# Kernel tuning notes

Hardware: AMD Instinct MI355X
Metric: run time of the kernel (lower is better)

## Reference

```python
import jax, jax.numpy as jnp
import numpy as np

DIM = 512
HEADS = 8
HEAD_DIM = DIM // HEADS
SCALE = HEAD_DIM ** -0.5
GROUP1 = np.array([2, 3, 5, 6, 1, 4, 0, 7, 8, 9, 14, 15, 11, 12, 10, 13])
GROUP2 = np.array([0, 1, 2, 3, 5, 6, 4, 7])
EPS = 1e-5


def setup_inputs() -> dict:
    key = jax.random.key(0)
    ks = jax.random.split(key, 6)
    B, N, C = 4096, 16, DIM
    x = jax.random.normal(ks[0], (B, N, C), dtype=jnp.float32)
    w_q = jax.random.normal(ks[1], (C, C), dtype=jnp.float32) * 0.02
    w_kv = jax.random.normal(ks[2], (2 * C, C), dtype=jnp.float32) * 0.02
    w_proj = jax.random.normal(ks[3], (C, C), dtype=jnp.float32) * 0.02
    b_proj = jax.random.normal(ks[4], (C,), dtype=jnp.float32) * 0.02
    gamma = jnp.ones((C,), dtype=jnp.float32)
    beta = jnp.zeros((C,), dtype=jnp.float32)
    return {"x": x, "w_q": w_q, "w_kv": w_kv, "w_proj": w_proj,
            "b_proj": b_proj, "gamma": gamma, "beta": beta}


def _layernorm(x, gamma, beta):
    mu = jnp.mean(x, axis=-1, keepdims=True)
    var = jnp.mean(jnp.square(x - mu), axis=-1, keepdims=True)
    return (x - mu) * jax.lax.rsqrt(var + EPS) * gamma + beta


def _avg_pool_pairs(x):
    # x: (B, L, C) -> (B, L//2, C), AvgPool1d(kernel=2, stride=2) over L
    return 0.5 * (x[:, 0::2] + x[:, 1::2])


def reference(x, w_q, w_kv, w_proj, b_proj, gamma, beta):
    B, N, C = x.shape
    q = (x @ w_q.T).reshape(B, N, HEADS, HEAD_DIM).transpose(0, 2, 1, 3)  # (B,H,N,d)
    # gather + avgpool preprocessing
    p1 = _avg_pool_pairs(x[:, GROUP1])  # (B, 8, C)
    p2 = _avg_pool_pairs(x[:, GROUP2])  # (B, 4, C)
    pools = jnp.concatenate([x, p1, p2], axis=1)  # (B, N+12, C)
    pools = _layernorm(pools, gamma, beta)
    M = pools.shape[1]
    kv = (pools @ w_kv.T).reshape(B, M, 2, HEADS, HEAD_DIM).transpose(2, 0, 3, 1, 4)
    k, v = kv[0], kv[1]  # (B,H,M,d)
    attn = jax.nn.softmax(jnp.einsum('bhnd,bhmd->bhnm', q, k) * SCALE, axis=-1)
    out = jnp.einsum('bhnm,bhmd->bhnd', attn, v)  # (B,H,N,d)
    out = out.transpose(0, 2, 1, 3).reshape(B, N, C)
    return out @ w_proj.T + b_proj
```

## Files before the change

kernel.cpp:

```cpp
#include <hip/hip_runtime.h>
#include <hip/hip_bf16.h>
#include <cstdint>
#include <cstddef>


using bf16 = __hip_bfloat16;

#define B_SZ   4096
#define NTOK   16
#define CDIM   512
#define MPOOL  28
#define NHEAD  8
#define HDIM   64
#define LN_EPS 1e-5f
#define ATT_SCALE 0.125f

typedef short bf16x8 __attribute__((ext_vector_type(8)));
typedef float f32x4  __attribute__((ext_vector_type(4)));

__constant__ int c_g1[16] = {2,3,5,6,1,4,0,7,8,9,14,15,11,12,10,13};
__constant__ int c_g2[8]  = {0,1,2,3,5,6,4,7};

__device__ __forceinline__ float us2f(unsigned short u) {
    return __uint_as_float(((unsigned)u) << 16);
}
__device__ __forceinline__ unsigned short f2b(float f) {
    unsigned u = __float_as_uint(f);
    return (unsigned short)((u + 0x7FFFu + ((u >> 16) & 1u)) >> 16);
}

__device__ __forceinline__ void lds_cp16(const void* g, void* l) {
    __builtin_amdgcn_global_load_lds(
        (const __attribute__((address_space(1))) void*)g,
        (__attribute__((address_space(3))) void*)l, 16, 0, 0);
}

__global__ __launch_bounds__(256) void f32_to_bf16_kernel(
    const float* __restrict__ src, bf16* __restrict__ dst, int n8)
{
    const int i = blockIdx.x * 256 + threadIdx.x;
    if (i >= n8) return;
    const float4* p = (const float4*)(src + (size_t)i * 8);
    float4 a = p[0], b = p[1];
    uint4 pk;
    pk.x = (unsigned)f2b(a.x) | ((unsigned)f2b(a.y) << 16);
    pk.y = (unsigned)f2b(a.z) | ((unsigned)f2b(a.w) << 16);
    pk.z = (unsigned)f2b(b.x) | ((unsigned)f2b(b.y) << 16);
    pk.w = (unsigned)f2b(b.z) | ((unsigned)f2b(b.w) << 16);
    *(uint4*)(dst + (size_t)i * 8) = pk;
}

__global__ __launch_bounds__(256) void pools_ln_kernel(
    const float* __restrict__ x, const float* __restrict__ gamma,
    const float* __restrict__ beta, bf16* __restrict__ pools,
    bf16* __restrict__ xb)
{
    const int wave = threadIdx.x >> 6;
    const int lane = threadIdx.x & 63;
    const int row  = blockIdx.x * 4 + wave;
    const int b = row / MPOOL;
    const int m = row % MPOOL;
    const float* xb_src = x + (size_t)b * NTOK * CDIM;
    const int c0 = lane * 8;

    float v[8];
    if (m < 16) {
        const float4* p = (const float4*)(xb_src + m * CDIM + c0);
        float4 a = p[0], c = p[1];
        v[0]=a.x; v[1]=a.y; v[2]=a.z; v[3]=a.w;
        v[4]=c.x; v[5]=c.y; v[6]=c.z; v[7]=c.w;
        uint4 pk;
        pk.x = (unsigned)f2b(v[0]) | ((unsigned)f2b(v[1]) << 16);
        pk.y = (unsigned)f2b(v[2]) | ((unsigned)f2b(v[3]) << 16);
        pk.z = (unsigned)f2b(v[4]) | ((unsigned)f2b(v[5]) << 16);
        pk.w = (unsigned)f2b(v[6]) | ((unsigned)f2b(v[7]) << 16);
        *(uint4*)(xb + (size_t)b * NTOK * CDIM + (size_t)m * CDIM + c0) = pk;
    } else {
        int r0, r1;
        if (m < 24) { int j = m - 16; r0 = c_g1[2*j]; r1 = c_g1[2*j+1]; }
        else        { int j = m - 24; r0 = c_g2[2*j]; r1 = c_g2[2*j+1]; }
        const float4* p0 = (const float4*)(xb_src + r0 * CDIM + c0);
        const float4* p1 = (const float4*)(xb_src + r1 * CDIM + c0);
        float4 a0 = p0[0], a1 = p0[1];
        float4 b0 = p1[0], b1 = p1[1];
        v[0]=0.5f*(a0.x+b0.x); v[1]=0.5f*(a0.y+b0.y);
        v[2]=0.5f*(a0.z+b0.z); v[3]=0.5f*(a0.w+b0.w);
        v[4]=0.5f*(a1.x+b1.x); v[5]=0.5f*(a1.y+b1.y);
        v[6]=0.5f*(a1.z+b1.z); v[7]=0.5f*(a1.w+b1.w);
    }

    float s = 0.f, sq = 0.f;
#pragma unroll
    for (int j = 0; j < 8; ++j) { s += v[j]; sq += v[j]*v[j]; }
#pragma unroll
    for (int off = 1; off < 64; off <<= 1) {
        s  += __shfl_xor(s,  off, 64);
        sq += __shfl_xor(sq, off, 64);
    }
    const float mu   = s * (1.f / CDIM);
    const float var  = sq * (1.f / CDIM) - mu * mu;
    const float rstd = rsqrtf(var + LN_EPS);

    unsigned short o[8];
#pragma unroll
    for (int j = 0; j < 8; ++j) {
        float g  = gamma[c0 + j];
        float bb = beta[c0 + j];
        o[j] = f2b((v[j] - mu) * rstd * g + bb);
    }
    uint4 pk;
    pk.x = (unsigned)o[0] | ((unsigned)o[1] << 16);
    pk.y = (unsigned)o[2] | ((unsigned)o[3] << 16);
    pk.z = (unsigned)o[4] | ((unsigned)o[5] << 16);
    pk.w = (unsigned)o[6] | ((unsigned)o[7] << 16);
    *(uint4*)(pools + (size_t)row * CDIM + c0) = pk;
}

template<bool OUT_BF16, bool BIAS, int NBLK>
__global__ __launch_bounds__(512, 2) void gemm256_kernel(
    const bf16* __restrict__ A, const bf16* __restrict__ W,
    const float* __restrict__ bias, void* __restrict__ Cptr, int Ncols)
{
    constexpr int K  = 512;
    constexpr int NT = K / 32;
    extern __shared__ __align__(16) char ring[];

    const int tid = threadIdx.x;
    const int wv = tid >> 6, ln = tid & 63;
    const int wr = wv >> 2, wc = wv & 3;
    const int fr = ln & 15, kb = ln >> 4;

    const int p  = blockIdx.x;
    const int o  = p >> 3;
    const int mb = (o / NBLK) * 8 + (p & 7);
    const int nb = o % NBLK;
    const size_t m0 = (size_t)mb * 256;
    const size_t n0 = (size_t)nb * 256;

    const int srow = wv * 16 + (ln >> 2);
    const int scol = (((ln & 3) * 16) ^ (((ln >> 3) & 3) << 4)) >> 1;
    const bf16* Asrc0 = A + (m0 + srow) * K + scol;
    const bf16* Asrc1 = A + (m0 + 128 + srow) * K + scol;
    const bf16* Wsrc0 = W + (n0 + srow) * K + scol;
    const bf16* Wsrc1 = W + (n0 + 128 + srow) * K + scol;
    char* const ringc = ring;

    const int aswz  = ((fr >> 1) & 3) << 4;
    const int a_off = (wr * 128 + fr) * 64 + ((kb * 16) ^ aswz);
    const int b_off = 16384 + (wc * 64 + fr) * 64 + ((kb * 16) ^ aswz);

    f32x4 acc[8][4];
#pragma unroll
    for (int i = 0; i < 8; ++i)
#pragma unroll
    for (int j = 0; j < 4; ++j)
        acc[i][j] = f32x4{0.f, 0.f, 0.f, 0.f};

    auto STAGE = [&](int t) {
        char* base = ringc + (t & 3) * 32768 + wv * 1024;
        const int ko = t * 32;
        lds_cp16(Asrc0 + ko, base);
        lds_cp16(Asrc1 + ko, base + 8192);
        lds_cp16(Wsrc0 + ko, base + 16384);
        lds_cp16(Wsrc1 + ko, base + 16384 + 8192);
    };

    STAGE(0);
    STAGE(1);
    asm volatile("s_waitcnt vmcnt(4)" ::: "memory");
    __builtin_amdgcn_s_barrier();

#pragma unroll 1
    for (int t = 0; t < NT; ++t) {
        if (t + 2 < NT) STAGE(t + 2);
        const char* sa = ringc + (t & 3) * 32768;

        bf16x8 af[8], bfr[4];
#pragma unroll
        for (int mi = 0; mi < 8; ++mi)
            af[mi] = *(const bf16x8*)(sa + a_off + mi * 1024);
#pragma unroll
        for (int nj = 0; nj < 4; ++nj)
            bfr[nj] = *(const bf16x8*)(sa + b_off + nj * 1024);

#pragma unroll
        for (int mi = 0; mi < 8; ++mi)
#pragma unroll
        for (int nj = 0; nj < 4; ++nj)
            acc[mi][nj] = __builtin_amdgcn_mfma_f32_16x16x32_bf16(
                af[mi], bfr[nj], acc[mi][nj], 0, 0, 0);

        if (t + 2 < NT) { asm volatile("s_waitcnt vmcnt(4)" ::: "memory"); }
        else            { asm volatile("s_waitcnt vmcnt(0)" ::: "memory"); }
        __builtin_amdgcn_s_barrier();
    }

    const int orow0 = wr * 128 + kb * 4;
    const int ocol0 = wc * 64 + fr;
    float bv[4];
#pragma unroll
    for (int nj = 0; nj < 4; ++nj)
        bv[nj] = BIAS ? bias[n0 + ocol0 + nj * 16] : 0.f;
#pragma unroll
    for (int mi = 0; mi < 8; ++mi) {
        const size_t rbase = m0 + orow0 + mi * 16;
#pragma unroll
        for (int r = 0; r < 4; ++r) {
            const size_t rowoff = (rbase + r) * (size_t)Ncols + n0 + ocol0;
#pragma unroll
            for (int nj = 0; nj < 4; ++nj) {
                float v = acc[mi][nj][r] + bv[nj];
                if (OUT_BF16)
                    ((unsigned short*)Cptr)[rowoff + nj * 16] = f2b(v);
                else
                    ((float*)Cptr)[rowoff + nj * 16] = v;
            }
        }
    }
}

__global__ __launch_bounds__(256) void attn_kernel(
    const bf16* __restrict__ q, const bf16* __restrict__ kv,
    bf16* __restrict__ att)
{
    __shared__ __align__(16) float qs[16][68];
    __shared__ __align__(16) float ks[28][68];
    __shared__ __align__(16) float vs[28][68];
    __shared__ float Ss[16][29];

    const int tid = threadIdx.x;
    const int b = blockIdx.x >> 3;
    const int h = blockIdx.x & 7;

    const bf16* qb  = q  + (size_t)b * NTOK * CDIM + h * HDIM;
    const bf16* kvb = kv + (size_t)b * MPOOL * (2 * CDIM) + h * HDIM;

    {
        const int n = tid >> 4, d4 = (tid & 15) << 2;
        ushort4 u = *(const ushort4*)(qb + n * CDIM + d4);
        qs[n][d4 + 0] = us2f(u.x); qs[n][d4 + 1] = us2f(u.y);
        qs[n][d4 + 2] = us2f(u.z); qs[n][d4 + 3] = us2f(u.w);
    }
    for (int e = tid; e < 448; e += 256) {
        const int m = e >> 4, d4 = (e & 15) << 2;
        ushort4 uk = *(const ushort4*)(kvb + (size_t)m * (2 * CDIM) + d4);
        ushort4 uv = *(const ushort4*)(kvb + (size_t)m * (2 * CDIM) + CDIM + d4);
        ks[m][d4 + 0] = us2f(uk.x); ks[m][d4 + 1] = us2f(uk.y);
        ks[m][d4 + 2] = us2f(uk.z); ks[m][d4 + 3] = us2f(uk.w);
        vs[m][d4 + 0] = us2f(uv.x); vs[m][d4 + 1] = us2f(uv.y);
        vs[m][d4 + 2] = us2f(uv.z); vs[m][d4 + 3] = us2f(uv.w);
    }
    __syncthreads();

    for (int e = tid; e < 448; e += 256) {
        const int n = e / MPOOL, m = e % MPOOL;
        float acc = 0.f;
#pragma unroll
        for (int d4 = 0; d4 < 64; d4 += 4) {
            float4 qq = *(const float4*)&qs[n][d4];
            float4 kk = *(const float4*)&ks[m][d4];
            acc += qq.x * kk.x + qq.y * kk.y + qq.z * kk.z + qq.w * kk.w;
        }
        Ss[n][m] = acc * ATT_SCALE;
    }
    __syncthreads();

    if (tid < 16) {
        const int n = tid;
        float mx = -1e30f;
        for (int m = 0; m < MPOOL; ++m) mx = fmaxf(mx, Ss[n][m]);
        float sum = 0.f;
        for (int m = 0; m < MPOOL; ++m) {
            float e = expf(Ss[n][m] - mx);
            Ss[n][m] = e; sum += e;
        }
        float inv = 1.f / sum;
        for (int m = 0; m < MPOOL; ++m) Ss[n][m] *= inv;
    }
    __syncthreads();

    {
        const int n = tid >> 4, d4 = (tid & 15) << 2;
        float o0 = 0.f, o1 = 0.f, o2 = 0.f, o3 = 0.f;
#pragma unroll
        for (int m = 0; m < MPOOL; ++m) {
            float p = Ss[n][m];
            float4 v4 = *(const float4*)&vs[m][d4];
            o0 = fmaf(p, v4.x, o0); o1 = fmaf(p, v4.y, o1);
            o2 = fmaf(p, v4.z, o2); o3 = fmaf(p, v4.w, o3);
        }
        uint2 st;
        st.x = (unsigned)f2b(o0) | ((unsigned)f2b(o1) << 16);
        st.y = (unsigned)f2b(o2) | ((unsigned)f2b(o3) << 16);
        *(uint2*)(att + (size_t)b * NTOK * CDIM + (size_t)n * CDIM + h * HDIM + d4) = st;
    }
}

extern "C" void kernel_launch(void* const* d_in, const int* in_sizes, int n_in,
                              void* d_out, int out_size, void* d_ws, size_t ws_size,
                              hipStream_t stream)
{
    const float* x      = (const float*)d_in[0];
    const float* w_q    = (const float*)d_in[1];
    const float* w_kv   = (const float*)d_in[2];
    const float* w_proj = (const float*)d_in[3];
    const float* b_proj = (const float*)d_in[4];
    const float* gamma  = (const float*)d_in[5];
    const float* beta   = (const float*)d_in[6];

    char* ws = (char*)d_ws;
    bf16* xb    = (bf16*)(ws);
    bf16* pools = (bf16*)(ws + 67108864ull);
    bf16* qbuf  = (bf16*)(ws + 67108864ull + 117440512ull);
    bf16* kvbuf = (bf16*)(ws + 67108864ull + 117440512ull + 67108864ull);
    bf16* wqb   = (bf16*)(ws + 67108864ull + 117440512ull + 67108864ull + 234881024ull);
    bf16* wkvb  = (bf16*)((char*)wqb + 524288ull);
    bf16* wpb   = (bf16*)((char*)wkvb + 1048576ull);
    bf16* atbuf = pools;

    hipFuncSetAttribute((const void*)gemm256_kernel<true, false, 2>,
                        hipFuncAttributeMaxDynamicSharedMemorySize, 131072);
    hipFuncSetAttribute((const void*)gemm256_kernel<true, false, 4>,
                        hipFuncAttributeMaxDynamicSharedMemorySize, 131072);
    hipFuncSetAttribute((const void*)gemm256_kernel<false, true, 2>,
                        hipFuncAttributeMaxDynamicSharedMemorySize, 131072);

    f32_to_bf16_kernel<<<128, 256, 0, stream>>>(w_q, wqb, 32768);
    f32_to_bf16_kernel<<<256, 256, 0, stream>>>(w_kv, wkvb, 65536);
    f32_to_bf16_kernel<<<128, 256, 0, stream>>>(w_proj, wpb, 32768);

    pools_ln_kernel<<<(B_SZ * MPOOL) / 4, 256, 0, stream>>>(x, gamma, beta, pools, xb);

    gemm256_kernel<true, false, 2><<<512, 512, 131072, stream>>>(
        xb, wqb, nullptr, (void*)qbuf, 512);

    gemm256_kernel<true, false, 4><<<1792, 512, 131072, stream>>>(
        pools, wkvb, nullptr, (void*)kvbuf, 1024);

    attn_kernel<<<B_SZ * NHEAD, 256, 0, stream>>>(qbuf, kvbuf, atbuf);

    gemm256_kernel<false, true, 2><<<512, 512, 131072, stream>>>(
        atbuf, wpb, b_proj, d_out, 512);
}
```

Before: 511.0 us.

## Rewrite attention as one-wave-per-head MFMA kernel with shuffle softmax

```diff
diff --git a/kernel.cpp b/kernel.cpp
--- a/kernel.cpp
+++ b/kernel.cpp
@@ -21,9 +21,6 @@
 __constant__ int c_g1[16] = {2,3,5,6,1,4,0,7,8,9,14,15,11,12,10,13};
 __constant__ int c_g2[8]  = {0,1,2,3,5,6,4,7};
 
-__device__ __forceinline__ float us2f(unsigned short u) {
-    return __uint_as_float(((unsigned)u) << 16);
-}
 __device__ __forceinline__ unsigned short f2b(float f) {
     unsigned u = __float_as_uint(f);
     return (unsigned short)((u + 0x7FFFu + ((u >> 16) & 1u)) >> 16);
@@ -223,76 +220,100 @@
     const bf16* __restrict__ q, const bf16* __restrict__ kv,
     bf16* __restrict__ att)
 {
-    __shared__ __align__(16) float qs[16][68];
-    __shared__ __align__(16) float ks[28][68];
-    __shared__ __align__(16) float vs[28][68];
-    __shared__ float Ss[16][29];
+    __shared__ unsigned short P_t[4][512];
 
     const int tid = threadIdx.x;
-    const int b = blockIdx.x >> 3;
-    const int h = blockIdx.x & 7;
-
-    const bf16* qb  = q  + (size_t)b * NTOK * CDIM + h * HDIM;
-    const bf16* kvb = kv + (size_t)b * MPOOL * (2 * CDIM) + h * HDIM;
+    const int wv = tid >> 6, ln = tid & 63;
+    const int fr = ln & 15, kb = ln >> 4;
+    const int wg = blockIdx.x * 4 + wv;
+    const int b = wg >> 3, h = wg & 7;
+
+    const bf16* qb = q  + (size_t)b * (NTOK * CDIM) + h * HDIM;
+    const bf16* kp = kv + (size_t)b * (MPOOL * 2 * CDIM) + h * HDIM;
+    const bf16* vp = kp + CDIM;
+
+    bf16x8 aq[2];
+#pragma unroll
+    for (int ks = 0; ks < 2; ++ks)
+        aq[ks] = *(const bf16x8*)(qb + fr * CDIM + ks * 32 + kb * 8);
+
+    bf16x8 bk[2][2];
+#pragma unroll
+    for (int mt = 0; mt < 2; ++mt)
+#pragma unroll
+        for (int ks = 0; ks < 2; ++ks)
+            bk[mt][ks] = *(const bf16x8*)(kp + (size_t)(mt * 16 + fr) * (2 * CDIM)
+                                             + ks * 32 + kb * 8);
+
+    const bf16* vlane = vp + (size_t)kb * 8 * (2 * CDIM) + fr;
+    bf16x8 bv[4];
+#pragma unroll
+    for (int dt = 0; dt < 4; ++dt)
+#pragma unroll
+        for (int j = 0; j < 8; ++j)
+            bv[dt][j] = *(const short*)(vlane + (size_t)j * (2 * CDIM) + dt * 16);
+
+    f32x4 st0 = {0.f, 0.f, 0.f, 0.f}, st1 = {0.f, 0.f, 0.f, 0.f};
+    st0 = __builtin_amdgcn_mfma_f32_16x16x32_bf16(aq[0], bk[0][0], st0, 0, 0, 0);
+    st0 = __builtin_amdgcn_mfma_f32_16x16x32_bf16(aq[1], bk[0][1], st0, 0, 0, 0);
+    st1 = __builtin_amdgcn_mfma_f32_16x16x32_bf16(aq[0], bk[1][0], st1, 0, 0, 0);
+    st1 = __builtin_amdgcn_mfma_f32_16x16x32_bf16(aq[1], bk[1][1], st1, 0, 0, 0);
+
+    const bool kmask = (fr >= MPOOL - 16);
+#pragma unroll
+    for (int r = 0; r < 4; ++r) {
+        st0[r] *= ATT_SCALE;
+        st1[r] = kmask ? -1e30f : st1[r] * ATT_SCALE;
+    }
+
+    float p0[4], p1[4];
+#pragma unroll
+    for (int r = 0; r < 4; ++r) {
+        float mx = fmaxf(st0[r], st1[r]);
+        mx = fmaxf(mx, __shfl_xor(mx, 1, 64));
+        mx = fmaxf(mx, __shfl_xor(mx, 2, 64));
+        mx = fmaxf(mx, __shfl_xor(mx, 4, 64));
+        mx = fmaxf(mx, __shfl_xor(mx, 8, 64));
+        float e0 = expf(st0[r] - mx);
+        float e1 = expf(st1[r] - mx);
+        float s = e0 + e1;
+        s += __shfl_xor(s, 1, 64);
+        s += __shfl_xor(s, 2, 64);
+        s += __shfl_xor(s, 4, 64);
+        s += __shfl_xor(s, 8, 64);
+        const float inv = 1.f / s;
+        p0[r] = e0 * inv;
+        p1[r] = e1 * inv;
+    }
 
     {
-        const int n = tid >> 4, d4 = (tid & 15) << 2;
-        ushort4 u = *(const ushort4*)(qb + n * CDIM + d4);
-        qs[n][d4 + 0] = us2f(u.x); qs[n][d4 + 1] = us2f(u.y);
-        qs[n][d4 + 2] = us2f(u.z); qs[n][d4 + 3] = us2f(u.w);
-    }
-    for (int e = tid; e < 448; e += 256) {
-        const int m = e >> 4, d4 = (e & 15) << 2;
-        ushort4 uk = *(const ushort4*)(kvb + (size_t)m * (2 * CDIM) + d4);
-        ushort4 uv = *(const ushort4*)(kvb + (size_t)m * (2 * CDIM) + CDIM + d4);
-        ks[m][d4 + 0] = us2f(uk.x); ks[m][d4 + 1] = us2f(uk.y);
-        ks[m][d4 + 2] = us2f(uk.z); ks[m][d4 + 3] = us2f(uk.w);
-        vs[m][d4 + 0] = us2f(uv.x); vs[m][d4 + 1] = us2f(uv.y);
-        vs[m][d4 + 2] = us2f(uv.z); vs[m][d4 + 3] = us2f(uv.w);
-    }
-    __syncthreads();
-
-    for (int e = tid; e < 448; e += 256) {
-        const int n = e / MPOOL, m = e % MPOOL;
-        float acc = 0.f;
-#pragma unroll
-        for (int d4 = 0; d4 < 64; d4 += 4) {
-            float4 qq = *(const float4*)&qs[n][d4];
-            float4 kk = *(const float4*)&ks[m][d4];
-            acc += qq.x * kk.x + qq.y * kk.y + qq.z * kk.z + qq.w * kk.w;
-        }
-        Ss[n][m] = acc * ATT_SCALE;
-    }
-    __syncthreads();
-
-    if (tid < 16) {
-        const int n = tid;
-        float mx = -1e30f;
-        for (int m = 0; m < MPOOL; ++m) mx = fmaxf(mx, Ss[n][m]);
-        float sum = 0.f;
-        for (int m = 0; m < MPOOL; ++m) {
-            float e = expf(Ss[n][m] - mx);
-            Ss[n][m] = e; sum += e;
-        }
-        float inv = 1.f / sum;
-        for (int m = 0; m < MPOOL; ++m) Ss[n][m] *= inv;
-    }
-    __syncthreads();
-
-    {
-        const int n = tid >> 4, d4 = (tid & 15) << 2;
-        float o0 = 0.f, o1 = 0.f, o2 = 0.f, o3 = 0.f;
-#pragma unroll
-        for (int m = 0; m < MPOOL; ++m) {
-            float p = Ss[n][m];
-            float4 v4 = *(const float4*)&vs[m][d4];
-            o0 = fmaf(p, v4.x, o0); o1 = fmaf(p, v4.y, o1);
-            o2 = fmaf(p, v4.z, o2); o3 = fmaf(p, v4.w, o3);
-        }
-        uint2 st;
-        st.x = (unsigned)f2b(o0) | ((unsigned)f2b(o1) << 16);
-        st.y = (unsigned)f2b(o2) | ((unsigned)f2b(o3) << 16);
-        *(uint2*)(att + (size_t)b * NTOK * CDIM + (size_t)n * CDIM + h * HDIM + d4) = st;
+        ushort4 w0, w1;
+        w0.x = f2b(p0[0]); w0.y = f2b(p0[1]); w0.z = f2b(p0[2]); w0.w = f2b(p0[3]);
+        w1.x = f2b(p1[0]); w1.y = f2b(p1[1]); w1.z = f2b(p1[2]); w1.w = f2b(p1[3]);
+        *(ushort4*)&P_t[wv][(fr)      * 16 + kb * 4] = w0;
+        *(ushort4*)&P_t[wv][(16 + fr) * 16 + kb * 4] = w1;
+    }
+    asm volatile("s_waitcnt lgkmcnt(0)" ::: "memory");
+
+    bf16x8 pa;
+#pragma unroll
+    for (int j = 0; j < 8; ++j)
+        pa[j] = (short)P_t[wv][(kb * 8 + j) * 16 + fr];
+
+    f32x4 o[4];
+#pragma unroll
+    for (int dt = 0; dt < 4; ++dt) {
+        o[dt] = f32x4{0.f, 0.f, 0.f, 0.f};
+        o[dt] = __builtin_amdgcn_mfma_f32_16x16x32_bf16(pa, bv[dt], o[dt], 0, 0, 0);
+    }
+
+    unsigned short* ob = (unsigned short*)(att + (size_t)b * (NTOK * CDIM) + h * HDIM);
+#pragma unroll
+    for (int r = 0; r < 4; ++r) {
+        const size_t nrow = (size_t)(kb * 4 + r) * CDIM;
+#pragma unroll
+        for (int dt = 0; dt < 4; ++dt)
+            ob[nrow + dt * 16 + fr] = f2b(o[dt][r]);
     }
 }
 
@@ -337,7 +358,7 @@
     gemm256_kernel<true, false, 4><<<1792, 512, 131072, stream>>>(
         pools, wkvb, nullptr, (void*)kvbuf, 1024);
 
-    attn_kernel<<<B_SZ * NHEAD, 256, 0, stream>>>(qbuf, kvbuf, atbuf);
+    attn_kernel<<<(B_SZ * NHEAD) / 4, 256, 0, stream>>>(qbuf, kvbuf, atbuf);
 
     gemm256_kernel<false, true, 2><<<512, 512, 131072, stream>>>(
         atbuf, wpb, b_proj, d_out, 512);
```

After: 432.3 us. 1.18x faster.
